# Kernel tuning notes

Measured on AMD Instinct MI355X. Metric: run time of the kernel, lower is better.

Reference implementation:

```python
import jax, jax.numpy as jnp
import numpy as np


def setup_inputs() -> dict:
    key = jax.random.key(0)
    k1, k2 = jax.random.split(key)
    B, T, H, D = 2, 2048, 16, 64          # batch, seq, heads, head_dim
    NUM_HASHES, NUM_BUCKETS = 4, 64
    hidden_states = jax.random.normal(k1, (B, T, H * D), dtype=jnp.float32)
    # equivalent of torch.randn rotations with fixed hash_seed
    random_rotations = jax.random.normal(k2, (H, D, NUM_HASHES, NUM_BUCKETS // 2), dtype=jnp.float32)
    return {"hidden_states": hidden_states, "random_rotations": random_rotations}


def reference(hidden_states, random_rotations):
    # hidden_states: [B, T, H*D]; random_rotations: [H, D, num_hashes, num_buckets//2]
    H, D, num_hashes, half = random_rotations.shape
    B, T, _ = hidden_states.shape
    # _split_hidden_size_dim: [B,T,H*D] -> [B,H,T,D]
    v = hidden_states.reshape(B, T, H, D).transpose(0, 2, 1, 3)
    # rotated: [B, H, num_hashes, T, num_buckets//2]
    rotated = jnp.einsum('bhtd,hdnr->bhntr', v, random_rotations)
    rotated = jnp.concatenate([rotated, -rotated], axis=-1)  # [..., num_buckets]
    buckets = jnp.argmax(rotated, axis=-1)                   # [B, H, num_hashes, T]
    b = buckets.transpose(0, 1, 3, 2)                        # [B, H, T, num_hashes]
    # m[b,h,i,j] = any_n (bucket_n(i) == bucket_n(j)); OR-accumulate over the
    # small fixed num_hashes axis to avoid a [B,H,T,T,num_hashes] intermediate.
    m = jnp.zeros((B, H, T, T), dtype=bool)
    for n in range(num_hashes):
        bn = b[..., n]
        m = m | (bn[:, :, :, None] == bn[:, :, None, :])
    return m
```

## Files before the change

### kernel.cpp

```cpp
#include <hip/hip_runtime.h>
#include <stdint.h>

#define BB 2
#define HH 16
#define TT 2048
#define DD 64
#define NHASH 4
#define NHALF 32

__global__ __launch_bounds__(256, 2) void lsh_buckets_kernel(
    const float* __restrict__ hs,
    const float* __restrict__ rot,
    uint32_t* __restrict__ words)
{
    __shared__ uint32_t lds[12288];
    float4* v4 = (float4*)lds;
    float4* r4 = (float4*)(lds + 4096);

    const int blk  = blockIdx.x;
    const int bh   = blk >> 5;
    const int tblk = blk & 31;
    const int b    = bh >> 4;
    const int h    = bh & 15;
    const int t0   = tblk * 64;
    const int tid  = threadIdx.x;
    const int n    = tid >> 6;
    const int lane = tid & 63;
    const int tg   = lane >> 3;
    const int rg   = lane & 7;

    #pragma unroll
    for (int p = 0; p < 4; ++p) {
        const int k  = tid + p * 256;
        const int t  = k >> 4;
        const int d4 = k & 15;
        const float4 f = ((const float4*)(hs + ((size_t)(b * TT + t0 + t)) * (HH * DD) + h * DD))[d4];
        v4[t * 16 + (d4 ^ (t >> 3))] = f;
    }
    {
        const float* rh = rot + (size_t)h * (DD * NHASH * NHALF);
        float* rf = (float*)r4;
        #pragma unroll
        for (int p = 0; p < 32; ++p) {
            const int g  = tid + p * 256;
            const int d  = g >> 7;
            const int nr = g & 127;
            const int nn = nr >> 5;
            const int r  = nr & 31;
            const int slot = (d >> 2) ^ (r >> 2);
            rf[((nn * 32 + r) * 16 + slot) * 4 + (d & 3)] = rh[g];
        }
    }
    __syncthreads();

    double acc[8][4];
    #pragma unroll
    for (int i = 0; i < 8; ++i)
        #pragma unroll
        for (int j = 0; j < 4; ++j) acc[i][j] = 0.0;

    const int vbase = tg * 8 * 16;
    const int rbase = (n * 32 + rg * 4) * 16;

    for (int s = 0; s < 16; ++s) {
        double rd[4][4];
        #pragma unroll
        for (int j = 0; j < 4; ++j) {
            const float4 rf = r4[rbase + j * 16 + (s ^ rg)];
            rd[j][0] = (double)rf.x; rd[j][1] = (double)rf.y;
            rd[j][2] = (double)rf.z; rd[j][3] = (double)rf.w;
        }
        #pragma unroll
        for (int i = 0; i < 8; ++i) {
            const float4 vf = v4[vbase + i * 16 + (s ^ tg)];
            const double v0 = (double)vf.x, v1 = (double)vf.y;
            const double v2 = (double)vf.z, v3 = (double)vf.w;
            #pragma unroll
            for (int j = 0; j < 4; ++j) {
                acc[i][j] += v0 * rd[j][0];
                acc[i][j] += v1 * rd[j][1];
                acc[i][j] += v2 * rd[j][2];
                acc[i][j] += v3 * rd[j][3];
            }
        }
    }

    __syncthreads();
    float*    vmaxL = (float*)lds;
    float*    vminL = (float*)(lds + 2304);
    uint32_t* imaxL = lds + 4608;
    uint32_t* iminL = lds + 6912;
    uint32_t* bkt   = lds + 9216;

    #pragma unroll
    for (int i = 0; i < 8; ++i) {
        const int t = tg * 8 + i;
        float fmx = -INFINITY; int imx = 0;
        float fmn =  INFINITY; int imn = 0;
        #pragma unroll
        for (int j = 0; j < 4; ++j) {
            const float f = (float)acc[i][j];
            const int   r = rg * 4 + j;
            if (f > fmx) { fmx = f; imx = r; }
            if (f < fmn) { fmn = f; imn = r; }
        }
        const int o = (n * 64 + t) * 9 + rg;
        vmaxL[o] = fmx; vminL[o] = fmn;
        imaxL[o] = (uint32_t)imx; iminL[o] = (uint32_t)imn;
    }
    __syncthreads();
    {
        const int nn = tid >> 6;
        const int t  = tid & 63;
        float fmx = -INFINITY; int imx = 0;
        float fmn =  INFINITY; int imn = 0;
        #pragma unroll
        for (int g = 0; g < 8; ++g) {
            const int o = (nn * 64 + t) * 9 + g;
            const float fx = vmaxL[o];
            const float fn = vminL[o];
            if (fx > fmx) { fmx = fx; imx = (int)imaxL[o]; }
            if (fn < fmn) { fmn = fn; imn = (int)iminL[o]; }
        }
        const uint32_t bucket = (fmx >= -fmn) ? (uint32_t)imx : (uint32_t)(NHALF + imn);
        bkt[nn * 64 + t] = bucket;
    }
    __syncthreads();
    if (tid < 64) {
        words[(size_t)bh * TT + t0 + tid] = bkt[tid]
                                          | (bkt[64  + tid] << 8)
                                          | (bkt[128 + tid] << 16)
                                          | (bkt[192 + tid] << 24);
    }
}

#define ROWS 8
__device__ __forceinline__ uint32_t eq_any_byte(uint32_t a, uint32_t b) {
    const uint32_t x = a ^ b;
    return ((x - 0x01010101u) & ~x & 0x80808080u) ? 1u : 0u;
}

__global__ __launch_bounds__(256) void lsh_mask_kernel(
    const uint32_t* __restrict__ words,
    uint4* __restrict__ out)
{
    const int bh  = blockIdx.x >> 8;
    const int i0  = (blockIdx.x & 255) * ROWS;
    const int tid = threadIdx.x;
    const uint32_t* wrow = words + (bh << 11);

    const uint4 wj0 = ((const uint4*)wrow)[tid];
    const uint4 wj1 = ((const uint4*)wrow)[tid + 256];

    #pragma unroll
    for (int k = 0; k < ROWS; ++k) {
        const uint32_t wi = wrow[i0 + k];
        uint4 r0, r1;
        r0.x = eq_any_byte(wi, wj0.x); r0.y = eq_any_byte(wi, wj0.y);
        r0.z = eq_any_byte(wi, wj0.z); r0.w = eq_any_byte(wi, wj0.w);
        r1.x = eq_any_byte(wi, wj1.x); r1.y = eq_any_byte(wi, wj1.y);
        r1.z = eq_any_byte(wi, wj1.z); r1.w = eq_any_byte(wi, wj1.w);
        uint4* op = out + (((size_t)((bh << 11) + i0 + k)) << 9);
        op[tid]       = r0;
        op[tid + 256] = r1;
    }
}

extern "C" void kernel_launch(void* const* d_in, const int* in_sizes, int n_in,
                              void* d_out, int out_size, void* d_ws, size_t ws_size,
                              hipStream_t stream) {
    const float* hs  = (const float*)d_in[0];
    const float* rot = (const float*)d_in[1];
    uint32_t* words  = (uint32_t*)d_ws;

    lsh_buckets_kernel<<<BB * HH * (TT / 64), 256, 0, stream>>>(hs, rot, words);
    lsh_mask_kernel<<<BB * HH * (TT / ROWS), 256, 0, stream>>>(words, (uint4*)d_out);
}
```

Baseline: 133.8 us.

## Enlarge bucket-kernel tile to 128 tokens and use nontemporal mask stores

The bucket kernel now handles 128 tokens per block, and each thread computes an 8x8 tile of double-precision dot products instead of 8x4, so each rotation load from LDS is reused across more work. The LDS swizzles and the two-stage argmax reduction are reworked to fit the new thread mapping. The mask kernel writes its output with nontemporal vector stores to keep the large boolean output from polluting the cache. The cost is more accumulator registers (64 doubles per thread), which may lower occupancy or cause spills, and half as many blocks in the bucket kernel.

```diff
diff --git a/kernel.cpp b/kernel.cpp
--- a/kernel.cpp
+++ b/kernel.cpp
@@ -8,34 +8,32 @@
 #define NHASH 4
 #define NHALF 32
 
+typedef uint32_t u32x4 __attribute__((ext_vector_type(4)));
+
 __global__ __launch_bounds__(256, 2) void lsh_buckets_kernel(
     const float* __restrict__ hs,
     const float* __restrict__ rot,
     uint32_t* __restrict__ words)
 {
-    __shared__ uint32_t lds[12288];
+    __shared__ uint32_t lds[16384];
     float4* v4 = (float4*)lds;
-    float4* r4 = (float4*)(lds + 4096);
+    float4* r4 = (float4*)(lds + 8192);
 
     const int blk  = blockIdx.x;
-    const int bh   = blk >> 5;
-    const int tblk = blk & 31;
+    const int bh   = blk >> 4;
+    const int tblk = blk & 15;
     const int b    = bh >> 4;
     const int h    = bh & 15;
-    const int t0   = tblk * 64;
+    const int t0   = tblk * 128;
     const int tid  = threadIdx.x;
-    const int n    = tid >> 6;
-    const int lane = tid & 63;
-    const int tg   = lane >> 3;
-    const int rg   = lane & 7;
 
     #pragma unroll
-    for (int p = 0; p < 4; ++p) {
+    for (int p = 0; p < 8; ++p) {
         const int k  = tid + p * 256;
         const int t  = k >> 4;
         const int d4 = k & 15;
         const float4 f = ((const float4*)(hs + ((size_t)(b * TT + t0 + t)) * (HH * DD) + h * DD))[d4];
-        v4[t * 16 + (d4 ^ (t >> 3))] = f;
+        v4[t * 16 + (d4 ^ ((t >> 3) & 7))] = f;
     }
     {
         const float* rh = rot + (size_t)h * (DD * NHASH * NHALF);
@@ -47,28 +45,36 @@
             const int nr = g & 127;
             const int nn = nr >> 5;
             const int r  = nr & 31;
-            const int slot = (d >> 2) ^ (r >> 2);
+            const int slot = (d >> 2) ^ (((r >> 3) & 3) | ((nn & 1) << 2));
             rf[((nn * 32 + r) * 16 + slot) * 4 + (d & 3)] = rh[g];
         }
     }
     __syncthreads();
 
-    double acc[8][4];
+    const int w     = tid >> 6;
+    const int lane  = tid & 63;
+    const int tg    = lane >> 3;
+    const int rg    = lane & 7;
+    const int thalf = (w >> 1) * 64;
+    const int nl    = (w & 1) * 2 + (rg >> 2);
+    const int r0    = (rg & 3) * 8;
+
+    double acc[8][8];
     #pragma unroll
     for (int i = 0; i < 8; ++i)
         #pragma unroll
-        for (int j = 0; j < 4; ++j) acc[i][j] = 0.0;
+        for (int j = 0; j < 8; ++j) acc[i][j] = 0.0;
 
-    const int vbase = tg * 8 * 16;
-    const int rbase = (n * 32 + rg * 4) * 16;
+    const int vbase = (thalf + tg * 8) * 16;
+    const int rbase = (nl * 32 + r0) * 16;
 
     for (int s = 0; s < 16; ++s) {
-        double rd[4][4];
+        double rd[8][4];
         #pragma unroll
-        for (int j = 0; j < 4; ++j) {
-            const float4 rf = r4[rbase + j * 16 + (s ^ rg)];
-            rd[j][0] = (double)rf.x; rd[j][1] = (double)rf.y;
-            rd[j][2] = (double)rf.z; rd[j][3] = (double)rf.w;
+        for (int j = 0; j < 8; ++j) {
+            const float4 f = r4[rbase + j * 16 + (s ^ rg)];
+            rd[j][0] = (double)f.x; rd[j][1] = (double)f.y;
+            rd[j][2] = (double)f.z; rd[j][3] = (double)f.w;
         }
         #pragma unroll
         for (int i = 0; i < 8; ++i) {
@@ -76,7 +82,7 @@
             const double v0 = (double)vf.x, v1 = (double)vf.y;
             const double v2 = (double)vf.z, v3 = (double)vf.w;
             #pragma unroll
-            for (int j = 0; j < 4; ++j) {
+            for (int j = 0; j < 8; ++j) {
                 acc[i][j] += v0 * rd[j][0];
                 acc[i][j] += v1 * rd[j][1];
                 acc[i][j] += v2 * rd[j][2];
@@ -86,51 +92,54 @@
     }
 
     __syncthreads();
-    float*    vmaxL = (float*)lds;
-    float*    vminL = (float*)(lds + 2304);
-    uint32_t* imaxL = lds + 4608;
-    uint32_t* iminL = lds + 6912;
-    uint32_t* bkt   = lds + 9216;
+    float*    pmax  = (float*)lds;
+    float*    pmin  = (float*)(lds + 2048);
+    uint32_t* pimax = lds + 4096;
+    uint32_t* pimin = lds + 6144;
+    uint32_t* bkt   = lds + 8192;
 
     #pragma unroll
     for (int i = 0; i < 8; ++i) {
-        const int t = tg * 8 + i;
         float fmx = -INFINITY; int imx = 0;
         float fmn =  INFINITY; int imn = 0;
         #pragma unroll
-        for (int j = 0; j < 4; ++j) {
+        for (int j = 0; j < 8; ++j) {
             const float f = (float)acc[i][j];
-            const int   r = rg * 4 + j;
+            const int   r = r0 + j;
             if (f > fmx) { fmx = f; imx = r; }
             if (f < fmn) { fmn = f; imn = r; }
         }
-        const int o = (n * 64 + t) * 9 + rg;
-        vmaxL[o] = fmx; vminL[o] = fmn;
-        imaxL[o] = (uint32_t)imx; iminL[o] = (uint32_t)imn;
+        const int o = (w * 8 + rg) * 64 + tg * 8 + i;
+        pmax[o] = fmx; pmin[o] = fmn;
+        pimax[o] = (uint32_t)imx; pimin[o] = (uint32_t)imn;
     }
     __syncthreads();
-    {
-        const int nn = tid >> 6;
-        const int t  = tid & 63;
+
+    #pragma unroll
+    for (int p = 0; p < 2; ++p) {
+        const int q    = tid + p * 256;
+        const int t128 = q & 127;
+        const int n    = q >> 7;
+        const int wsrc = (t128 >> 6) * 2 + (n >> 1);
+        const int gh   = (n & 1) * 4;
         float fmx = -INFINITY; int imx = 0;
         float fmn =  INFINITY; int imn = 0;
         #pragma unroll
-        for (int g = 0; g < 8; ++g) {
-            const int o = (nn * 64 + t) * 9 + g;
-            const float fx = vmaxL[o];
-            const float fn = vminL[o];
-            if (fx > fmx) { fmx = fx; imx = (int)imaxL[o]; }
-            if (fn < fmn) { fmn = fn; imn = (int)iminL[o]; }
+        for (int g = 0; g < 4; ++g) {
+            const int o = (wsrc * 8 + gh + g) * 64 + (t128 & 63);
+            const float fx = pmax[o], fn = pmin[o];
+            if (fx > fmx) { fmx = fx; imx = (int)pimax[o]; }
+            if (fn < fmn) { fmn = fn; imn = (int)pimin[o]; }
         }
-        const uint32_t bucket = (fmx >= -fmn) ? (uint32_t)imx : (uint32_t)(NHALF + imn);
-        bkt[nn * 64 + t] = bucket;
+        bkt[t128 * 4 + n] = (fmx >= -fmn) ? (uint32_t)imx : (uint32_t)(NHALF + imn);
     }
     __syncthreads();
-    if (tid < 64) {
-        words[(size_t)bh * TT + t0 + tid] = bkt[tid]
-                                          | (bkt[64  + tid] << 8)
-                                          | (bkt[128 + tid] << 16)
-                                          | (bkt[192 + tid] << 24);
+
+    if (tid < 128) {
+        words[(size_t)bh * TT + t0 + tid] = bkt[tid * 4 + 0]
+                                          | (bkt[tid * 4 + 1] << 8)
+                                          | (bkt[tid * 4 + 2] << 16)
+                                          | (bkt[tid * 4 + 3] << 24);
     }
 }
 
@@ -142,7 +151,7 @@
 
 __global__ __launch_bounds__(256) void lsh_mask_kernel(
     const uint32_t* __restrict__ words,
-    uint4* __restrict__ out)
+    uint32_t* __restrict__ out)
 {
     const int bh  = blockIdx.x >> 8;
     const int i0  = (blockIdx.x & 255) * ROWS;
@@ -155,14 +164,14 @@
     #pragma unroll
     for (int k = 0; k < ROWS; ++k) {
         const uint32_t wi = wrow[i0 + k];
-        uint4 r0, r1;
+        u32x4 r0, r1;
         r0.x = eq_any_byte(wi, wj0.x); r0.y = eq_any_byte(wi, wj0.y);
         r0.z = eq_any_byte(wi, wj0.z); r0.w = eq_any_byte(wi, wj0.w);
         r1.x = eq_any_byte(wi, wj1.x); r1.y = eq_any_byte(wi, wj1.y);
         r1.z = eq_any_byte(wi, wj1.z); r1.w = eq_any_byte(wi, wj1.w);
-        uint4* op = out + (((size_t)((bh << 11) + i0 + k)) << 9);
-        op[tid]       = r0;
-        op[tid + 256] = r1;
+        uint32_t* op = out + (((size_t)((bh << 11) + i0 + k)) << 11);
+        __builtin_nontemporal_store(r0, (u32x4*)(op) + tid);
+        __builtin_nontemporal_store(r1, (u32x4*)(op) + tid + 256);
     }
 }
 
@@ -173,6 +182,6 @@
     const float* rot = (const float*)d_in[1];
     uint32_t* words  = (uint32_t*)d_ws;
 
-    lsh_buckets_kernel<<<BB * HH * (TT / 64), 256, 0, stream>>>(hs, rot, words);
-    lsh_mask_kernel<<<BB * HH * (TT / ROWS), 256, 0, stream>>>(words, (uint4*)d_out);
+    lsh_buckets_kernel<<<BB * HH * (TT / 128), 256, 0, stream>>>(hs, rot, words);
+    lsh_mask_kernel<<<BB * HH * (TT / ROWS), 256, 0, stream>>>(words, (uint32_t*)d_out);
 }
```

After: 152.7 us. 14.2% more time.
